# Kernel tuning notes

Hardware: AMD Instinct MI355X
Metric: run time of the kernel (lower is better)

## Reference

```python
import jax, jax.numpy as jnp
import numpy as np
from itertools import product

B = 2
X, Y, Z = 96, 96, 192          # voxel grid (x, y, t)
NPB = 300_000                   # occupied voxels per batch item
PX, PY, PZ = X // 2, Y // 2, Z // 4  # pooled grid (kernel/stride [2,2,4])
CIN, COUT, KVOL, NCONV = 32, 64, 27, 2
EPS = 1e-5


def _build_maps():
    """Builds sparse coordinates, maxpool segment ids and 3x3x3 conv kernel maps
    (gather/scatter index pairs per kernel offset), mirroring MinkowskiEngine's
    coordinate manager."""
    rng = np.random.default_rng(0)
    coords = []
    for b in range(B):
        lin = rng.choice(X * Y * Z, NPB, replace=False)
        x = lin // (Y * Z)
        y = (lin // Z) % Y
        z = lin % Z
        coords.append(np.stack([np.full(NPB, b), x, y, z], 1))
    c = np.concatenate(coords).astype(np.int64)  # [N,4] (b,x,y,z)
    # max-pool coord map: out coord = (x//2, y//2, z//4)
    pk = ((c[:, 0] * PX + c[:, 1] // 2) * PY + c[:, 2] // 2) * PZ + c[:, 3] // 4
    uniq, inv = np.unique(pk, return_inverse=True)
    M = len(uniq)
    pz = uniq % PZ
    py = (uniq // PZ) % PY
    px = (uniq // (PZ * PY)) % PX
    pb = uniq // (PZ * PY * PX)
    lut = np.full(B * PX * PY * PZ, -1, np.int64)
    lut[uniq] = np.arange(M)
    ins, outs = [], []
    for dx, dy, dz in product((-1, 0, 1), repeat=3):
        nx, ny, nz = px + dx, py + dy, pz + dz
        ok = (nx >= 0) & (nx < PX) & (ny >= 0) & (ny < PY) & (nz >= 0) & (nz < PZ)
        nk = ((pb * PX + np.clip(nx, 0, PX - 1)) * PY + np.clip(ny, 0, PY - 1)) * PZ + np.clip(nz, 0, PZ - 1)
        j = np.where(ok, lut[nk], -1)
        sel = j >= 0
        ins.append(j[sel])
        outs.append(np.arange(M)[sel])
    L = max(len(a) for a in ins)
    ci = np.full((KVOL, L), M, np.int64)  # pad -> index M (zero row)
    co = np.full((KVOL, L), M, np.int64)  # pad -> dummy out row M (dropped)
    for k in range(KVOL):
        ci[k, : len(ins[k])] = ins[k]
        co[k, : len(outs[k])] = outs[k]
    return inv.astype(np.int64), ci, co, M


def setup_inputs() -> dict:
    key = jax.random.key(0)
    ks = jax.random.split(key, 4)
    pool_seg, ci, co, M = _build_maps()
    N = B * NPB
    feats = jax.random.normal(ks[0], (N, CIN), jnp.float32)
    Wd = jax.random.normal(ks[1], (CIN, COUT), jnp.float32) / np.sqrt(CIN)
    W1 = jax.random.normal(ks[2], (KVOL, COUT, COUT), jnp.float32) / np.sqrt(KVOL * COUT)
    W2 = jax.random.normal(ks[3], (KVOL, COUT, COUT), jnp.float32) / np.sqrt(KVOL * COUT)
    ones = jnp.ones((COUT,), jnp.float32)
    zeros = jnp.zeros((COUT,), jnp.float32)
    return {
        "feats": feats, "Wd": Wd,
        "g0": ones, "b0": zeros,
        "W1": W1, "g1": ones, "b1": zeros,
        "W2": W2, "g2": ones, "b2": zeros,
        "pool_seg": jnp.asarray(pool_seg),
        "conv_in": jnp.asarray(ci), "conv_out": jnp.asarray(co),
        "num_pooled": int(M),
    }


def _bn(h, g, b):
    # training-mode batch norm over all sparse points (biased variance, eps=1e-5)
    m = h.mean(0)
    v = jnp.mean((h - m) ** 2, 0)
    return (h - m) * (g / jnp.sqrt(v + EPS)) + b


def _sparse_conv(h, W, conv_in, conv_out, M):
    # gather-GEMM-scatter over 27 kernel offsets (MinkowskiConvolution, bias=False)
    C = W.shape[-1]
    hp = jnp.concatenate([h, jnp.zeros((1, h.shape[1]), h.dtype)])  # zero pad row
    out = jnp.zeros((M + 1, C), h.dtype)
    for k in range(W.shape[0]):
        out = out.at[conv_out[k]].add(hp[conv_in[k]] @ W[k])
    return out[:M]


def reference(feats, Wd, g0, b0, W1, g1, b1, W2, g2, b2,
              pool_seg, conv_in, conv_out, num_pooled):
    # down_conv (1x1, bias=False) -> BN -> ELU
    h = jax.nn.elu(_bn(feats @ Wd, g0, b0))
    # MinkowskiMaxPooling kernel=stride=[2,2,4] == segment max over pooled cells
    down = jax.ops.segment_max(h, pool_seg, num_segments=num_pooled)
    # nConvs LUConv blocks: ELU(BN(conv3x3x3(x)))
    o = down
    for W, g, b in ((W1, g1, b1), (W2, g2, b2)):
        o = jax.nn.elu(_bn(_sparse_conv(o, W, conv_in, conv_out, num_pooled), g, b))
    # residual add + ELU
    return jax.nn.elu(o + down)
```

## Files before the change

### kernel.cpp

```cpp
#include <hip/hip_runtime.h>
#include <math.h>

#define CIN  32
#define COUT 64
#define KVOL 27
#define EPSF 1e-5f

typedef __attribute__((ext_vector_type(8))) short          short8;
typedef __attribute__((ext_vector_type(8))) unsigned short u16x8;
typedef __attribute__((ext_vector_type(4))) float          float4v;

__device__ __forceinline__ float eluf(float x) { return x > 0.f ? x : expm1f(x); }

__device__ __forceinline__ unsigned short f2bf(float x) {
    unsigned u = __float_as_uint(x);
    unsigned r = (u + 0x7FFFu + ((u >> 16) & 1u)) >> 16;
    return (unsigned short)r;
}
__device__ __forceinline__ unsigned pk2bf(float lo, float hi) {
    return (unsigned)f2bf(lo) | ((unsigned)f2bf(hi) << 16);
}
__device__ __forceinline__ float bf2f(unsigned short h) {
    return __uint_as_float(((unsigned)h) << 16);
}

__device__ __forceinline__ void gload_lds16(const unsigned short* src, unsigned short* dst) {
    __builtin_amdgcn_global_load_lds(
        (const __attribute__((address_space(1))) unsigned int*)(const void*)src,
        (__attribute__((address_space(3))) unsigned int*)(void*)dst, 16, 0, 0);
}

__global__ void prep_kernel(const float* __restrict__ W1, const float* __restrict__ W2,
                            const float* __restrict__ Wd,
                            unsigned short* __restrict__ Wt1, unsigned short* __restrict__ Wt2,
                            unsigned short* __restrict__ Wdt,
                            const int* __restrict__ pool_seg, int* __restrict__ cnt,
                            int* __restrict__ bucket, int N,
                            const int* __restrict__ conv_out, const int* __restrict__ conv_in,
                            int* __restrict__ nbrT, int L, int M, int nbB, int nbL)
{
    int b = blockIdx.x, t = threadIdx.x;
    if (b < 55) {
        if (b == 54) {
            for (int e = t; e < CIN * COUT; e += 256) {
                int i = e >> 6, c = e & 63;
                Wdt[c * CIN + i] = f2bf(Wd[e]);
            }
            return;
        }
        const float* W = (b < 27) ? W1 : W2;
        unsigned short* Wt = (b < 27) ? Wt1 : Wt2;
        int k = (b < 27) ? b : b - 27;
        const float* src = W + (size_t)k * (COUT * COUT);
        unsigned short* dst = Wt + (size_t)k * (COUT * COUT);
        for (int e = t; e < COUT * COUT; e += 256) {
            int i = e >> 6, c = e & 63;
            dst[c * COUT + i] = f2bf(src[e]);
        }
        return;
    }
    b -= 55;
    if (b < nbB) {
        int j = b * 256 + t;
        if (j < N) {
            int s = pool_seg[j];
            int pos = atomicAdd(&cnt[s], 1);
            bucket[(size_t)s * 16 + pos] = j;
        }
        return;
    }
    b -= nbB;
    int k = b / nbL, blk = b - k * nbL;
    int idx = blk * 256 + t;
    if (idx < L) {
        int e = k * L + idx;
        int j = conv_out[e];
        if (j < M) nbrT[(size_t)k * M + j] = conv_in[e];
    }
}

__global__ __launch_bounds__(256) void gemm_t_kernel(
    const float* __restrict__ feats, const unsigned short* __restrict__ Wdt,
    int N, unsigned short* __restrict__ t_bf, float* __restrict__ red0)
{
    __shared__ float red_s[64];
    __shared__ float red_q[64];
    __shared__ __align__(16) unsigned short xpose[4][16 * 64];
    int t = threadIdx.x;
    if (t < 64) { red_s[t] = 0.f; red_q[t] = 0.f; }
    __syncthreads();

    int w = t >> 6, lane = t & 63, l15 = lane & 15, quad = lane >> 4;
    int p = lane >> 2, qq = lane & 3;

    short8 aw[4];
    #pragma unroll
    for (int mt = 0; mt < 4; ++mt)
        aw[mt] = *(const short8*)(Wdt + (size_t)(16 * mt + l15) * CIN + quad * 8);

    float s1[16], sq[16];
    #pragma unroll
    for (int e = 0; e < 16; ++e) { s1[e] = 0.f; sq[e] = 0.f; }

    int numTiles = (N + 15) >> 4;
    int stride = gridDim.x * 4;
    int tile = blockIdx.x * 4 + w;

    float4 c0 = make_float4(0.f, 0.f, 0.f, 0.f), c1 = c0;
    {
        int pt = tile * 16 + l15;
        if (tile < numTiles && pt < N) {
            const float4* s = (const float4*)(feats + (size_t)pt * CIN + quad * 8);
            c0 = s[0]; c1 = s[1];
        }
    }

    while (tile < numTiles) {
        int nt = tile + stride;
        float4 n0 = make_float4(0.f, 0.f, 0.f, 0.f), n1 = n0;
        {
            int npt = nt * 16 + l15;
            if (nt < numTiles && npt < N) {
                const float4* s = (const float4*)(feats + (size_t)npt * CIN + quad * 8);
                n0 = s[0]; n1 = s[1];
            }
        }
        union { short8 v; unsigned u[4]; } b;
        b.u[0] = pk2bf(c0.x, c0.y);
        b.u[1] = pk2bf(c0.z, c0.w);
        b.u[2] = pk2bf(c1.x, c1.y);
        b.u[3] = pk2bf(c1.z, c1.w);

        float4v acc[4];
        #pragma unroll
        for (int mt = 0; mt < 4; ++mt)
            acc[mt] = __builtin_amdgcn_mfma_f32_16x16x32_bf16(
                aw[mt], b.v, (float4v){0.f, 0.f, 0.f, 0.f}, 0, 0, 0);

        {
            char* xb = (char*)xpose[w];
            #pragma unroll
            for (int mt = 0; mt < 4; ++mt) {
                uint2 o;
                o.x = pk2bf(acc[mt][0], acc[mt][1]);
                o.y = pk2bf(acc[mt][2], acc[mt][3]);
                *(uint2*)(xb + l15 * 128 + (((mt * 4 + quad) ^ l15) * 8)) = o;
            }
            int pt2 = tile * 16 + p;
            if (pt2 < N) {
                uint2 d0 = *(uint2*)(xb + p * 128 + (((qq * 4 + 0) ^ p) * 8));
                uint2 d1 = *(uint2*)(xb + p * 128 + (((qq * 4 + 1) ^ p) * 8));
                uint2 d2 = *(uint2*)(xb + p * 128 + (((qq * 4 + 2) ^ p) * 8));
                uint2 d3 = *(uint2*)(xb + p * 128 + (((qq * 4 + 3) ^ p) * 8));
                uint4 o0 = make_uint4(d0.x, d0.y, d1.x, d1.y);
                uint4 o1 = make_uint4(d2.x, d2.y, d3.x, d3.y);
                *(uint4*)(t_bf + (size_t)pt2 * COUT + qq * 16) = o0;
                *(uint4*)(t_bf + (size_t)pt2 * COUT + qq * 16 + 8) = o1;
            }
        }

        #pragma unroll
        for (int mt = 0; mt < 4; ++mt)
            #pragma unroll
            for (int e = 0; e < 4; ++e) {
                float v = acc[mt][e];
                s1[mt * 4 + e] += v; sq[mt * 4 + e] += v * v;
            }
        c0 = n0; c1 = n1;
        tile = nt;
    }

    #pragma unroll
    for (int m = 1; m <= 8; m <<= 1) {
        #pragma unroll
        for (int e = 0; e < 16; ++e) {
            s1[e] += __shfl_xor(s1[e], m);
            sq[e] += __shfl_xor(sq[e], m);
        }
    }
    if (l15 == 0) {
        #pragma unroll
        for (int e = 0; e < 16; ++e) {
            int ch = (e >> 2) * 16 + quad * 4 + (e & 3);
            atomicAdd(&red_s[ch], s1[e]);
            atomicAdd(&red_q[ch], sq[e]);
        }
    }
    __syncthreads();
    float* dst = red0 + (size_t)(blockIdx.x & 3) * 128;
    if (t < 64)       atomicAdd(&dst[t], red_s[t]);
    else if (t < 128) atomicAdd(&dst[t], red_q[t - 64]);
}

__global__ __launch_bounds__(256) void pool_max_kernel(
    const unsigned short* __restrict__ t_bf,
    const int* __restrict__ cnt, const int* __restrict__ bucket,
    const float* __restrict__ red0, const float* __restrict__ g0,
    const float* __restrict__ b0,
    unsigned short* __restrict__ down_bf, int M, int N)
{
    __shared__ float sc_s[64], sh_s[64];
    __shared__ int bkt_s[16][16];
    __shared__ int cnt_s[16];
    int t = threadIdx.x;
    if (t < 64) {
        float s = 0.f, q2 = 0.f;
        #pragma unroll
        for (int i = 0; i < 4; ++i) { s += red0[i * 128 + t]; q2 += red0[i * 128 + 64 + t]; }
        float m = s / (float)N;
        float var = q2 / (float)N - m * m;
        float sc = g0[t] / sqrtf(var + EPSF);
        sc_s[t] = sc;
        sh_s[t] = b0[t] - m * sc;
    }
    int sb0 = blockIdx.x * 16;
    {
        int j = sb0 * 16 + t;
        ((int*)bkt_s)[t] = (j < M * 16) ? bucket[j] : 0;
        if (t < 16) cnt_s[t] = (sb0 + t < M) ? cnt[sb0 + t] : 0;
    }
    __syncthreads();

    int sl = t >> 4, cg = t & 15;
    int s = sb0 + sl;
    if (s >= M) return;
    int n = cnt_s[sl];
    float4 mx = make_float4(-INFINITY, -INFINITY, -INFINITY, -INFINITY);
    float4 mn = make_float4( INFINITY,  INFINITY,  INFINITY,  INFINITY);
    for (int p = 0; p < n; ++p) {
        int idx = bkt_s[sl][p];
        ushort4 v = *(const ushort4*)(t_bf + (size_t)idx * COUT + cg * 4);
        float f0 = bf2f(v.x), f1 = bf2f(v.y), f2 = bf2f(v.z), f3 = bf2f(v.w);
        mx.x = fmaxf(mx.x, f0); mn.x = fminf(mn.x, f0);
        mx.y = fmaxf(mx.y, f1); mn.y = fminf(mn.y, f1);
        mx.z = fmaxf(mx.z, f2); mn.z = fminf(mn.z, f2);
        mx.w = fmaxf(mx.w, f3); mn.w = fminf(mn.w, f3);
    }
    int c0 = cg * 4;
    float scx = sc_s[c0], scy = sc_s[c0 + 1], scz = sc_s[c0 + 2], scw = sc_s[c0 + 3];
    float shx = sh_s[c0], shy = sh_s[c0 + 1], shz = sh_s[c0 + 2], shw = sh_s[c0 + 3];
    ushort4 o;
    o.x = f2bf(eluf(scx * (scx >= 0.f ? mx.x : mn.x) + shx));
    o.y = f2bf(eluf(scy * (scy >= 0.f ? mx.y : mn.y) + shy));
    o.z = f2bf(eluf(scz * (scz >= 0.f ? mx.z : mn.z) + shz));
    o.w = f2bf(eluf(scw * (scw >= 0.f ? mx.w : mn.w) + shw));
    *(ushort4*)(down_bf + (size_t)s * COUT + c0) = o;
}

__global__ __launch_bounds__(256) void bn_elu_cvt_kernel(
    const unsigned short* __restrict__ o1b, const float* __restrict__ red,
    const float* __restrict__ g, const float* __restrict__ bb,
    unsigned short* __restrict__ o1t, int n4, int M)
{
    __shared__ float sc_s[64], sh_s[64];
    int t = threadIdx.x;
    if (t < 64) {
        float m = red[t] / (float)M;
        float var = red[64 + t] / (float)M - m * m;
        float sc = g[t] / sqrtf(var + EPSF);
        sc_s[t] = sc;
        sh_s[t] = bb[t] - m * sc;
    }
    __syncthreads();
    int i = blockIdx.x * 256 + t;
    if (i < n4) {
        ushort4 v = ((const ushort4*)o1b)[i];
        int c0 = (i & 15) * 4;
        ushort4 o;
        o.x = f2bf(eluf(bf2f(v.x) * sc_s[c0]     + sh_s[c0]));
        o.y = f2bf(eluf(bf2f(v.y) * sc_s[c0 + 1] + sh_s[c0 + 1]));
        o.z = f2bf(eluf(bf2f(v.z) * sc_s[c0 + 2] + sh_s[c0 + 2]));
        o.w = f2bf(eluf(bf2f(v.w) * sc_s[c0 + 3] + sh_s[c0 + 3]));
        ((ushort4*)o1t)[i] = o;
    }
}

__global__ __launch_bounds__(256) void final_kernel(
    float* __restrict__ out, const unsigned short* __restrict__ o2b,
    const unsigned short* __restrict__ down_bf,
    const float* __restrict__ red, const float* __restrict__ g,
    const float* __restrict__ bb, int n4, int M)
{
    __shared__ float sc_s[64], sh_s[64];
    int t = threadIdx.x;
    if (t < 64) {
        float m = red[t] / (float)M;
        float var = red[64 + t] / (float)M - m * m;
        float sc = g[t] / sqrtf(var + EPSF);
        sc_s[t] = sc;
        sh_s[t] = bb[t] - m * sc;
    }
    __syncthreads();
    int i = blockIdx.x * 256 + t;
    if (i < n4) {
        ushort4 v = ((const ushort4*)o2b)[i];
        ushort4 d = ((const ushort4*)down_bf)[i];
        int c0 = (i & 15) * 4;
        float4 o;
        o.x = eluf(eluf(bf2f(v.x) * sc_s[c0]     + sh_s[c0])     + bf2f(d.x));
        o.y = eluf(eluf(bf2f(v.y) * sc_s[c0 + 1] + sh_s[c0 + 1]) + bf2f(d.y));
        o.z = eluf(eluf(bf2f(v.z) * sc_s[c0 + 2] + sh_s[c0 + 2]) + bf2f(d.z));
        o.w = eluf(eluf(bf2f(v.w) * sc_s[c0 + 3] + sh_s[c0 + 3]) + bf2f(d.w));
        ((float4*)out)[i] = o;
    }
}

__global__ __launch_bounds__(512, 4) void conv_mfma_kernel(
    const unsigned short* __restrict__ in,
    const unsigned short* __restrict__ Wt,
    const int* __restrict__ nbrT, int M,
    unsigned short* __restrict__ outb, float* __restrict__ red_out)
{
    __shared__ __align__(16) unsigned short A_lds[2][256 * 64];
    __shared__ __align__(16) unsigned short W_lds[2][64 * 64];
    int t = threadIdx.x;

    int nwg = gridDim.x;
    int q = nwg >> 3, r = nwg & 7;
    int xcd = blockIdx.x & 7, pos = blockIdx.x >> 3;
    int sb = (xcd < r ? xcd * (q + 1) : r * (q + 1) + (xcd - r) * q) + pos;
    int base = sb * 256;

    int w = t >> 6, lane = t & 63, l15 = lane & 15, quad = lane >> 4;
    int ar8 = lane >> 3, ac = lane & 7;

    float4v acc[2][4];
    #pragma unroll
    for (int s = 0; s < 2; ++s)
        #pragma unroll
        for (int n = 0; n < 4; ++n)
            acc[s][n] = (float4v){0.f, 0.f, 0.f, 0.f};

    auto LOADIDX = [&](int k, int* e) {
        #pragma unroll
        for (int i = 0; i < 4; ++i) {
            int rr = (w << 5) + (i << 3) + ar8;
            int j = base + rr;
            int idx = nbrT[(size_t)k * M + (j < M ? j : 0)];
            e[i] = (j < M && idx >= 0) ? idx : M;
        }
    };
    auto STAGE = [&](int buf, const int* e, int kw) {
        unsigned short* An = A_lds[buf];
        unsigned short* Wn = W_lds[buf];
        #pragma unroll
        for (int i = 0; i < 4; ++i) {
            int rr = (w << 5) + (i << 3) + ar8;
            gload_lds16(in + (size_t)e[i] * COUT + ((ac ^ (rr & 7)) * 8),
                        An + (w << 11) + (i << 9));
        }
        int wr = (w << 3) + ar8;
        gload_lds16(Wt + (size_t)kw * (COUT * COUT) + wr * COUT + ((ac ^ (wr & 7)) * 8),
                    Wn + (w << 9));
    };

    int eC[4], eN[4];
    LOADIDX(0, eC);
    STAGE(0, eC, 0);
    LOADIDX(1, eC);
    __syncthreads();

    for (int k = 0; k < KVOL; ++k) {
        bool pf = (k + 1 < KVOL);
        if (pf) {
            STAGE((k + 1) & 1, eC, k + 1);
            if (k + 2 < KVOL) LOADIDX(k + 2, eN);
        }
        __builtin_amdgcn_sched_barrier(0);

        const unsigned short* Ab = A_lds[k & 1];
        const unsigned short* Wb = W_lds[k & 1];
        #pragma unroll
        for (int kk = 0; kk < 64; kk += 32) {
            int slb = quad + (kk >> 3);
            int r0 = 32 * w + l15;
            short8 a0 = *(const short8*)(Ab + r0 * 64 + ((slb ^ (r0 & 7)) * 8));
            int r1 = r0 + 16;
            short8 a1 = *(const short8*)(Ab + r1 * 64 + ((slb ^ (r1 & 7)) * 8));
            #pragma unroll
            for (int n = 0; n < 4; ++n) {
                int rb = 16 * n + l15;
                short8 b = *(const short8*)(Wb + rb * 64 + ((slb ^ (rb & 7)) * 8));
                acc[0][n] = __builtin_amdgcn_mfma_f32_16x16x32_bf16(a0, b, acc[0][n], 0, 0, 0);
                acc[1][n] = __builtin_amdgcn_mfma_f32_16x16x32_bf16(a1, b, acc[1][n], 0, 0, 0);
            }
        }

        if (pf) {
            #pragma unroll
            for (int i = 0; i < 4; ++i) eC[i] = eN[i];
        }
        __syncthreads();
    }

    #pragma unroll
    for (int s = 0; s < 2; ++s) {
        int row = base + 32 * w + 16 * s + quad * 4;
        #pragma unroll
        for (int n = 0; n < 4; ++n) {
            int c = 16 * n + l15;
            #pragma unroll
            for (int e = 0; e < 4; ++e)
                if (row + e < M)
                    outb[(size_t)(row + e) * COUT + c] = f2bf(acc[s][n][e]);
        }
    }

    float* red_s = (float*)(W_lds[0]);
    float* red_q = red_s + 64;
    if (t < 128) red_s[t] = 0.f;
    __syncthreads();
    #pragma unroll
    for (int n = 0; n < 4; ++n) {
        float s1 = 0.f, sq = 0.f;
        #pragma unroll
        for (int s = 0; s < 2; ++s)
            #pragma unroll
            for (int e = 0; e < 4; ++e) { float v = acc[s][n][e]; s1 += v; sq += v * v; }
        s1 += __shfl_xor(s1, 16); sq += __shfl_xor(sq, 16);
        s1 += __shfl_xor(s1, 32); sq += __shfl_xor(sq, 32);
        if (quad == 0) {
            atomicAdd(&red_s[16 * n + l15], s1);
            atomicAdd(&red_q[16 * n + l15], sq);
        }
    }
    __syncthreads();
    if (t < 64)       atomicAdd(&red_out[t], red_s[t]);
    else if (t < 128) atomicAdd(&red_out[t], red_q[t - 64]);
}

extern "C" void kernel_launch(void* const* d_in, const int* in_sizes, int n_in,
                              void* d_out, int out_size, void* d_ws, size_t ws_size,
                              hipStream_t stream)
{
    (void)n_in; (void)ws_size;
    const float* feats    = (const float*)d_in[0];
    const float* Wd       = (const float*)d_in[1];
    const float* g0       = (const float*)d_in[2];
    const float* b0       = (const float*)d_in[3];
    const float* W1       = (const float*)d_in[4];
    const float* g1       = (const float*)d_in[5];
    const float* b1       = (const float*)d_in[6];
    const float* W2       = (const float*)d_in[7];
    const float* g2       = (const float*)d_in[8];
    const float* b2       = (const float*)d_in[9];
    const int*   pool_seg = (const int*)d_in[10];
    const int*   conv_in  = (const int*)d_in[11];
    const int*   conv_out = (const int*)d_in[12];

    int N = in_sizes[0] / CIN;
    int M = out_size / COUT;
    int L = in_sizes[11] / KVOL;

    char* ws = (char*)d_ws;
    size_t off = 0;
    auto alloc = [&](size_t bytes) -> void* {
        void* p = ws + off;
        off = (off + bytes + 255) & ~(size_t)255;
        return p;
    };
    unsigned short* down_bf = (unsigned short*)alloc((size_t)(M + 1) * COUT * 2);
    unsigned short* o1b     = (unsigned short*)alloc((size_t)M * COUT * 2);
    unsigned short* o1t     = (unsigned short*)alloc((size_t)(M + 1) * COUT * 2);
    unsigned short* o2b     = (unsigned short*)alloc((size_t)M * COUT * 2);
    unsigned short* t_bf    = (unsigned short*)alloc((size_t)N * COUT * 2);
    int*            nbrT    = (int*)alloc((size_t)KVOL * M * 4);
    unsigned short* Wt1     = (unsigned short*)alloc((size_t)KVOL * COUT * COUT * 2);
    unsigned short* Wt2     = (unsigned short*)alloc((size_t)KVOL * COUT * COUT * 2);
    unsigned short* Wdt     = (unsigned short*)alloc((size_t)CIN * COUT * 2);
    int*            bucket  = (int*)alloc((size_t)(M + 16) * 16 * 4);
    int*            cnt     = (int*)alloc((size_t)M * 4);
    float*          red     = (float*)alloc((size_t)768 * 4);
    float* red0 = red, *red1 = red + 512, *red2 = red + 640;

    hipMemsetAsync(nbrT, 0xFF, (size_t)KVOL * M * 4, stream);
    hipMemsetAsync(cnt, 0, (size_t)((char*)(red + 768) - (char*)cnt), stream);
    hipMemsetAsync(down_bf + (size_t)M * COUT, 0, COUT * 2, stream);
    hipMemsetAsync(o1t + (size_t)M * COUT, 0, COUT * 2, stream);

    int nbB = (N + 255) / 256, nbL = (L + 255) / 256;
    prep_kernel<<<55 + nbB + nbL * KVOL, 256, 0, stream>>>(
        W1, W2, Wd, Wt1, Wt2, Wdt, pool_seg, cnt, bucket, N,
        conv_out, conv_in, nbrT, L, M, nbB, nbL);
    gemm_t_kernel<<<1024, 256, 0, stream>>>(feats, Wdt, N, t_bf, red0);
    pool_max_kernel<<<(M + 15) / 16, 256, 0, stream>>>(
        t_bf, cnt, bucket, red0, g0, b0, down_bf, M, N);

    int cblocks = (M + 255) / 256;
    int n4 = (M * COUT) / 4;
    conv_mfma_kernel<<<cblocks, 512, 0, stream>>>(down_bf, Wt1, nbrT, M, o1b, red1);
    bn_elu_cvt_kernel<<<(n4 + 255) / 256, 256, 0, stream>>>(o1b, red1, g1, b1, o1t, n4, M);
    conv_mfma_kernel<<<cblocks, 512, 0, stream>>>(o1t, Wt2, nbrT, M, o2b, red2);
    final_kernel<<<(n4 + 255) / 256, 256, 0, stream>>>(
        (float*)d_out, o2b, down_bf, red2, g2, b2, n4, M);
}
```

Measured before the change: 472.8 us.

## Rework conv gather pipeline with partial vmcnt waits and raw barriers

```diff
diff --git a/kernel.cpp b/kernel.cpp
--- a/kernel.cpp
+++ b/kernel.cpp
@@ -354,22 +354,24 @@
                     Wn + (w << 9));
     };
 
-    int eC[4], eN[4];
-    LOADIDX(0, eC);
-    STAGE(0, eC, 0);
-    LOADIDX(1, eC);
-    __syncthreads();
-
-    for (int k = 0; k < KVOL; ++k) {
-        bool pf = (k + 1 < KVOL);
-        if (pf) {
-            STAGE((k + 1) & 1, eC, k + 1);
-            if (k + 2 < KVOL) LOADIDX(k + 2, eN);
-        }
+    int e0[4], eA[4], eB[4];
+    LOADIDX(0, e0);
+    LOADIDX(1, eA);
+    STAGE(0, e0, 0);
+
+    auto STEP = [&](int k, int* u, int* x) {
+        int k2 = (k + 2 < KVOL) ? k + 2 : KVOL - 1;
+        LOADIDX(k2, x);
+        int k1 = (k + 1 < KVOL) ? k + 1 : KVOL - 1;
+        STAGE((k + 1) & 1, u, k1);
+        __builtin_amdgcn_sched_barrier(0);
+        asm volatile("s_waitcnt vmcnt(9)" ::: "memory");
+        __builtin_amdgcn_s_barrier();
         __builtin_amdgcn_sched_barrier(0);
 
         const unsigned short* Ab = A_lds[k & 1];
         const unsigned short* Wb = W_lds[k & 1];
+        __builtin_amdgcn_s_setprio(1);
         #pragma unroll
         for (int kk = 0; kk < 64; kk += 32) {
             int slb = quad + (kk >> 3);
@@ -385,12 +387,14 @@
                 acc[1][n] = __builtin_amdgcn_mfma_f32_16x16x32_bf16(a1, b, acc[1][n], 0, 0, 0);
             }
         }
-
-        if (pf) {
-            #pragma unroll
-            for (int i = 0; i < 4; ++i) eC[i] = eN[i];
-        }
-        __syncthreads();
+        __builtin_amdgcn_s_setprio(0);
+        __builtin_amdgcn_sched_barrier(0);
+        __builtin_amdgcn_s_barrier();
+    };
+
+    for (int k = 0; k < KVOL; k += 2) {
+        STEP(k, eA, eB);
+        if (k + 1 < KVOL) STEP(k + 1, eB, eA);
     }
 
     #pragma unroll
```

Measured after the change: 485.4 us. +2.7%, slower.

## Merge prep and 1x1 GEMM kernels into one launch, drop small memsets

Applied to the files above, without the earlier changes.

```diff
diff --git a/kernel.cpp b/kernel.cpp
--- a/kernel.cpp
+++ b/kernel.cpp
@@ -30,24 +30,24 @@
         (__attribute__((address_space(3))) unsigned int*)(void*)dst, 16, 0, 0);
 }
 
-__global__ void prep_kernel(const float* __restrict__ W1, const float* __restrict__ W2,
-                            const float* __restrict__ Wd,
-                            unsigned short* __restrict__ Wt1, unsigned short* __restrict__ Wt2,
-                            unsigned short* __restrict__ Wdt,
-                            const int* __restrict__ pool_seg, int* __restrict__ cnt,
-                            int* __restrict__ bucket, int N,
-                            const int* __restrict__ conv_out, const int* __restrict__ conv_in,
-                            int* __restrict__ nbrT, int L, int M, int nbB, int nbL)
-{
+__global__ __launch_bounds__(256) void mega_kernel(
+    const float* __restrict__ W1, const float* __restrict__ W2,
+    unsigned short* __restrict__ Wt1, unsigned short* __restrict__ Wt2,
+    const int* __restrict__ pool_seg, int* __restrict__ cnt,
+    int* __restrict__ bucket, int N,
+    const int* __restrict__ conv_out, const int* __restrict__ conv_in,
+    int* __restrict__ nbrT, int L, int M, int nbB, int nbL,
+    const float* __restrict__ feats, const float* __restrict__ Wd,
+    unsigned short* __restrict__ t_bf, float* __restrict__ red0,
+    unsigned short* __restrict__ down_bf, unsigned short* __restrict__ o1t,
+    int gemmBase)
+{
+    __shared__ float red_s[64];
+    __shared__ float red_q[64];
+    __shared__ __align__(16) unsigned short xpose[4][16 * 64];
     int b = blockIdx.x, t = threadIdx.x;
-    if (b < 55) {
-        if (b == 54) {
-            for (int e = t; e < CIN * COUT; e += 256) {
-                int i = e >> 6, c = e & 63;
-                Wdt[c * CIN + i] = f2bf(Wd[e]);
-            }
-            return;
-        }
+
+    if (b < 54) {
         const float* W = (b < 27) ? W1 : W2;
         unsigned short* Wt = (b < 27) ? Wt1 : Wt2;
         int k = (b < 27) ? b : b - 27;
@@ -59,9 +59,12 @@
         }
         return;
     }
-    b -= 55;
-    if (b < nbB) {
-        int j = b * 256 + t;
+    if (b < 54 + nbB) {
+        if (b == 54) {
+            if (t < 64)            down_bf[(size_t)M * COUT + t] = 0;
+            else if (t < 128)      o1t[(size_t)M * COUT + (t - 64)] = 0;
+        }
+        int j = (b - 54) * 256 + t;
         if (j < N) {
             int s = pool_seg[j];
             int pos = atomicAdd(&cnt[s], 1);
@@ -69,24 +72,19 @@
         }
         return;
     }
-    b -= nbB;
-    int k = b / nbL, blk = b - k * nbL;
-    int idx = blk * 256 + t;
-    if (idx < L) {
-        int e = k * L + idx;
-        int j = conv_out[e];
-        if (j < M) nbrT[(size_t)k * M + j] = conv_in[e];
-    }
-}
-
-__global__ __launch_bounds__(256) void gemm_t_kernel(
-    const float* __restrict__ feats, const unsigned short* __restrict__ Wdt,
-    int N, unsigned short* __restrict__ t_bf, float* __restrict__ red0)
-{
-    __shared__ float red_s[64];
-    __shared__ float red_q[64];
-    __shared__ __align__(16) unsigned short xpose[4][16 * 64];
-    int t = threadIdx.x;
+    if (b < gemmBase) {
+        int bb = b - 54 - nbB;
+        int k = bb / nbL, blk = bb - k * nbL;
+        int idx = blk * 256 + t;
+        if (idx < L) {
+            int e = k * L + idx;
+            int j = conv_out[e];
+            if (j < M) nbrT[(size_t)k * M + j] = conv_in[e];
+        }
+        return;
+    }
+
+    int gb = b - gemmBase;
     if (t < 64) { red_s[t] = 0.f; red_q[t] = 0.f; }
     __syncthreads();
 
@@ -95,16 +93,19 @@
 
     short8 aw[4];
     #pragma unroll
-    for (int mt = 0; mt < 4; ++mt)
-        aw[mt] = *(const short8*)(Wdt + (size_t)(16 * mt + l15) * CIN + quad * 8);
+    for (int mt = 0; mt < 4; ++mt) {
+        #pragma unroll
+        for (int j = 0; j < 8; ++j)
+            aw[mt][j] = (short)f2bf(Wd[(quad * 8 + j) * COUT + 16 * mt + l15]);
+    }
 
     float s1[16], sq[16];
     #pragma unroll
     for (int e = 0; e < 16; ++e) { s1[e] = 0.f; sq[e] = 0.f; }
 
     int numTiles = (N + 15) >> 4;
-    int stride = gridDim.x * 4;
-    int tile = blockIdx.x * 4 + w;
+    int stride = 1024 * 4;
+    int tile = gb * 4 + w;
 
     float4 c0 = make_float4(0.f, 0.f, 0.f, 0.f), c1 = c0;
     {
@@ -125,17 +126,17 @@
                 n0 = s[0]; n1 = s[1];
             }
         }
-        union { short8 v; unsigned u[4]; } b;
-        b.u[0] = pk2bf(c0.x, c0.y);
-        b.u[1] = pk2bf(c0.z, c0.w);
-        b.u[2] = pk2bf(c1.x, c1.y);
-        b.u[3] = pk2bf(c1.z, c1.w);
+        union { short8 v; unsigned u[4]; } bb;
+        bb.u[0] = pk2bf(c0.x, c0.y);
+        bb.u[1] = pk2bf(c0.z, c0.w);
+        bb.u[2] = pk2bf(c1.x, c1.y);
+        bb.u[3] = pk2bf(c1.z, c1.w);
 
         float4v acc[4];
         #pragma unroll
         for (int mt = 0; mt < 4; ++mt)
             acc[mt] = __builtin_amdgcn_mfma_f32_16x16x32_bf16(
-                aw[mt], b.v, (float4v){0.f, 0.f, 0.f, 0.f}, 0, 0, 0);
+                aw[mt], bb.v, (float4v){0.f, 0.f, 0.f, 0.f}, 0, 0, 0);
 
         {
             char* xb = (char*)xpose[w];
@@ -187,7 +188,7 @@
         }
     }
     __syncthreads();
-    float* dst = red0 + (size_t)(blockIdx.x & 3) * 128;
+    float* dst = red0 + (size_t)(gb & 3) * 128;
     if (t < 64)       atomicAdd(&dst[t], red_s[t]);
     else if (t < 128) atomicAdd(&dst[t], red_q[t - 64]);
 }
@@ -467,7 +468,6 @@
     int*            nbrT    = (int*)alloc((size_t)KVOL * M * 4);
     unsigned short* Wt1     = (unsigned short*)alloc((size_t)KVOL * COUT * COUT * 2);
     unsigned short* Wt2     = (unsigned short*)alloc((size_t)KVOL * COUT * COUT * 2);
-    unsigned short* Wdt     = (unsigned short*)alloc((size_t)CIN * COUT * 2);
     int*            bucket  = (int*)alloc((size_t)(M + 16) * 16 * 4);
     int*            cnt     = (int*)alloc((size_t)M * 4);
     float*          red     = (float*)alloc((size_t)768 * 4);
@@ -475,14 +475,13 @@
 
     hipMemsetAsync(nbrT, 0xFF, (size_t)KVOL * M * 4, stream);
     hipMemsetAsync(cnt, 0, (size_t)((char*)(red + 768) - (char*)cnt), stream);
-    hipMemsetAsync(down_bf + (size_t)M * COUT, 0, COUT * 2, stream);
-    hipMemsetAsync(o1t + (size_t)M * COUT, 0, COUT * 2, stream);
 
     int nbB = (N + 255) / 256, nbL = (L + 255) / 256;
-    prep_kernel<<<55 + nbB + nbL * KVOL, 256, 0, stream>>>(
-        W1, W2, Wd, Wt1, Wt2, Wdt, pool_seg, cnt, bucket, N,
-        conv_out, conv_in, nbrT, L, M, nbB, nbL);
-    gemm_t_kernel<<<1024, 256, 0, stream>>>(feats, Wdt, N, t_bf, red0);
+    int gemmBase = 54 + nbB + nbL * KVOL;
+    mega_kernel<<<gemmBase + 1024, 256, 0, stream>>>(
+        W1, W2, Wt1, Wt2, pool_seg, cnt, bucket, N,
+        conv_out, conv_in, nbrT, L, M, nbB, nbL,
+        feats, Wd, t_bf, red0, down_bf, o1t, gemmBase);
     pool_max_kernel<<<(M + 15) / 16, 256, 0, stream>>>(
         t_bf, cnt, bucket, red0, g0, b0, down_bf, M, N);
 
```

New measurement: 486.1 us. +2.8%, slower.
